# Kernel optimization log

Hardware: AMD Instinct MI355X
Metric: run time of the kernel (lower is better)

Reference implementation:

```python
import jax, jax.numpy as jnp
import numpy as np

# Static architecture of the decoded CNN (matches init_kwargs index_dict)
KERNEL_NO = [64, 128, 256]
KERNEL_SIZE = [9, 9, 9]
CH_IN = [3, 64, 128]
IDX_START = [0, 1792, 75648]
I_DIM = 370816  # last slice's last index + 1
D_MODEL = 512
BATCH = 128
N_LAYERS = len(KERNEL_NO)


def _build_slices():
    """Replicates DebedderNeuron.get_kernel_slices(); per-layer int32 index matrix [K_l, L_l]."""
    sl = []
    for idx in range(N_LAYERS):
        rows = []
        for kd in range(KERNEL_NO[idx]):
            s = IDX_START[idx] + kd * KERNEL_SIZE[idx] * CH_IN[idx]
            e = s + KERNEL_SIZE[idx] * CH_IN[idx]
            bias = IDX_START[idx] + KERNEL_NO[idx] * KERNEL_SIZE[idx] * CH_IN[idx] + kd
            ik = list(range(s, e)) + [bias]
            if idx < N_LAYERS - 1:
                for kn in range(KERNEL_NO[idx + 1]):
                    ns = (IDX_START[idx + 1] + kd * KERNEL_SIZE[idx + 1]
                          + kn * CH_IN[idx + 1] * KERNEL_SIZE[idx + 1])
                    ik.extend(range(ns, ns + KERNEL_SIZE[idx + 1]))
            rows.append(ik)
        sl.append(jnp.asarray(np.array(rows, dtype=np.int32)))
    return sl

IDX = _build_slices()  # lengths per row: [1180, 2881, 1153]


def setup_inputs() -> dict:
    key = jax.random.key(0)
    ks = jax.random.split(key, 7)
    dims = [int(IDX[l].shape[1]) for l in range(N_LAYERS)]
    inp = {"x": jax.random.normal(ks[0], (BATCH, sum(KERNEL_NO), D_MODEL), jnp.float32)}
    for l in range(N_LAYERS):
        inp[f"W{l}"] = jax.random.normal(ks[1 + 2 * l], (D_MODEL, dims[l]), jnp.float32) * 0.02
        inp[f"b{l}"] = jax.random.normal(ks[2 + 2 * l], (dims[l],), jnp.float32) * 0.02
    return inp


def reference(x, W0, b0, W1, b1, W2, b2):
    # One shared Linear per CNN layer (as in the torch module); batch all kernels of a
    # layer into a single GEMM, then scatter-add into the flat weight vector y.
    Ws = [W0, W1, W2]
    bs = [b0, b1, b2]
    y = jnp.zeros((x.shape[0], I_DIM), x.dtype)
    off = 0
    for l in range(N_LAYERS):
        K = KERNEL_NO[l]
        yt = jnp.einsum('bkd,di->bki', x[:, off:off + K], Ws[l]) + bs[l]  # [B, K_l, L_l]
        y = y.at[:, IDX[l]].add(yt)  # overlapping scatter-add, matches sequential += in torch
        off += K
    # middle layers are written twice (own slice + previous layer's extension) -> halve
    y = y.at[:, IDX_START[1]:IDX_START[-1]].multiply(0.5)
    return y
```

## Files before the change

### kernel.cpp

```cpp
#include <hip/hip_runtime.h>
#include <cstdint>

typedef short short8 __attribute__((ext_vector_type(8)));
typedef float f32x4 __attribute__((ext_vector_type(4)));

#define LDS_AS3(p) ((__attribute__((address_space(3))) unsigned*)(p))
#define GLB_AS1(p) ((const __attribute__((address_space(1))) unsigned*)(p))

__device__ inline unsigned bfpack(float a, float b) {
    union { float f; unsigned u; } ua, ub;
    ua.f = a; ub.f = b;
    unsigned lo = (ua.u + 0x7FFFu + ((ua.u >> 16) & 1u)) >> 16;
    unsigned hi = (ub.u + 0x7FFFu + ((ub.u >> 16) & 1u)) & 0xFFFF0000u;
    return lo | hi;
}

__global__ __launch_bounds__(256)
void cvt_x(const float* __restrict__ X, unsigned short* __restrict__ XB)
{
    const int g = blockIdx.x * 256 + threadIdx.x;
    const float4 v0 = *(const float4*)(X + (size_t)g * 8);
    const float4 v1 = *(const float4*)(X + (size_t)g * 8 + 4);
    uint4 u;
    u.x = bfpack(v0.x, v0.y); u.y = bfpack(v0.z, v0.w);
    u.z = bfpack(v1.x, v1.y); u.w = bfpack(v1.z, v1.w);
    *(uint4*)(XB + (size_t)g * 8) = u;
}

template <int N>
__global__ __launch_bounds__(256)
void cvt_w(const float* __restrict__ W, unsigned short* __restrict__ WT)
{
    const int g = blockIdx.x * 256 + threadIdx.x;
    if (g >= N * 64) return;
    const int n = g % N, d8 = g / N;
    const float* p = W + (size_t)d8 * 8 * N + n;
    uint4 u;
    u.x = bfpack(p[0],             p[(size_t)N]);
    u.y = bfpack(p[2 * (size_t)N], p[3 * (size_t)N]);
    u.z = bfpack(p[4 * (size_t)N], p[5 * (size_t)N]);
    u.w = bfpack(p[6 * (size_t)N], p[7 * (size_t)N]);
    *(uint4*)(WT + (size_t)n * 512 + d8 * 8) = u;
}

template <int MODE>
__global__ __launch_bounds__(256)
void gemm_scatter(const unsigned short* __restrict__ XB,
                  const unsigned short* __restrict__ WT,
                  const float* __restrict__ BIAS, float* __restrict__ Y)
{
    constexpr int K_L  = (MODE == 0) ? 64 : (MODE == 1) ? 128 : 256;
    constexpr int LOGK = (MODE == 0) ? 6  : (MODE == 1) ? 7   : 8;
    constexpr int N    = (MODE == 0) ? 1180 : (MODE == 1) ? 2881 : 1153;
    constexpr int XOFF = (MODE == 0) ? 0 : (MODE == 1) ? 64 : 192;
    constexpr int NT   = (N + 127) / 128;

    __shared__ __align__(16) unsigned short lA[2][128 * 32];
    __shared__ __align__(16) unsigned short lB[2][128 * 32];

    const int t    = threadIdx.x;
    const int lane = t & 63;
    const int wave = t >> 6;
    const int wr   = wave >> 1, wc = wave & 1;

    const int cpx = (int)gridDim.x >> 3;
    const int wg  = (blockIdx.x & 7) * cpx + (blockIdx.x >> 3);
    const int nt  = wg % NT;
    const int mt  = wg / NT;
    const int m0  = mt * 128;
    const int n0  = nt * 128;

    f32x4 acc[4][4] = {};

    auto stage = [&](int buf, int kk) {
        #pragma unroll
        for (int i = 0; i < 2; ++i) {
            const int cidx = i * 256 + t;
            const int row  = cidx >> 2;
            const int kgl  = (cidx & 3) ^ ((row >> 1) & 3);
            const int m    = m0 + row;
            const int b    = m >> LOGK;
            const int kd   = m & (K_L - 1);
            const unsigned short* gp =
                XB + ((size_t)(b * 448 + XOFF + kd) << 9) + kk + kgl * 8;
            __builtin_amdgcn_global_load_lds(GLB_AS1(gp), LDS_AS3(&lA[buf][cidx * 8]), 16, 0, 0);
        }
        #pragma unroll
        for (int i = 0; i < 2; ++i) {
            const int cidx = i * 256 + t;
            const int row  = cidx >> 2;
            const int kgl  = (cidx & 3) ^ ((row >> 1) & 3);
            int gc = n0 + row; if (gc > N - 1) gc = N - 1;
            const unsigned short* gp = WT + (size_t)gc * 512 + kk + kgl * 8;
            __builtin_amdgcn_global_load_lds(GLB_AS1(gp), LDS_AS3(&lB[buf][cidx * 8]), 16, 0, 0);
        }
    };

    stage(0, 0);
    __syncthreads();

    int cur = 0;
    #pragma unroll 1
    for (int ks = 0; ks < 16; ++ks) {
        const int nxt = cur ^ 1;
        if (ks < 15) stage(nxt, (ks + 1) * 32);

        const int kgl  = lane >> 4;
        const int lr16 = lane & 15;
        short8 af[4], bfr[4];
        #pragma unroll
        for (int mi = 0; mi < 4; ++mi) {
            const int row = wr * 64 + mi * 16 + lr16;
            af[mi] = *(const short8*)(&lA[cur][(row * 4 + (kgl ^ ((row >> 1) & 3))) * 8]);
        }
        #pragma unroll
        for (int ni = 0; ni < 4; ++ni) {
            const int row = wc * 64 + ni * 16 + lr16;
            bfr[ni] = *(const short8*)(&lB[cur][(row * 4 + (kgl ^ ((row >> 1) & 3))) * 8]);
        }
        #pragma unroll
        for (int mi = 0; mi < 4; ++mi)
            #pragma unroll
            for (int ni = 0; ni < 4; ++ni)
                acc[mi][ni] = __builtin_amdgcn_mfma_f32_16x16x32_bf16(
                    af[mi], bfr[ni], acc[mi][ni], 0, 0, 0);

        __syncthreads();
        cur = nxt;
    }

    const int lr = lane & 15;
    const int lq = lane >> 4;
    #pragma unroll
    for (int ni = 0; ni < 4; ++ni) {
        const int n = n0 + wc * 64 + ni * 16 + lr;
        if (n >= N) continue;
        const float bias = BIAS[n];
        #pragma unroll
        for (int mi = 0; mi < 4; ++mi) {
            #pragma unroll
            for (int r = 0; r < 4; ++r) {
                const int m  = m0 + wr * 64 + mi * 16 + lq * 4 + r;
                const int b  = m >> LOGK;
                const int kd = m & (K_L - 1);
                const float v = acc[mi][ni][r] + bias;
                float* yb = Y + (size_t)b * 370816;
                if (MODE == 0) {
                    if (n < 27)       yb[kd * 27 + n] = v;
                    else if (n == 27) yb[1728 + kd]   = v;
                    else {
                        int tt = n - 28, kn = tt / 9, j = tt - kn * 9;
                        yb[1792 + kn * 576 + kd * 9 + j] = 0.5f * v;
                    }
                } else if (MODE == 1) {
                    if (n < 576)       yb[1792 + kd * 576 + n] += 0.5f * v;
                    else if (n == 576) yb[75520 + kd] = 0.5f * v;
                    else {
                        int tt = n - 577, kn = tt / 9, j = tt - kn * 9;
                        yb[75648 + kn * 1152 + kd * 9 + j] = v;
                    }
                } else {
                    if (n < 1152) yb[75648 + kd * 1152 + n] += v;
                    else          yb[370560 + kd] = v;
                }
            }
        }
    }
}

extern "C" void kernel_launch(void* const* d_in, const int* in_sizes, int n_in,
                              void* d_out, int out_size, void* d_ws, size_t ws_size,
                              hipStream_t stream)
{
    const float* x  = (const float*)d_in[0];
    const float* W0 = (const float*)d_in[1];
    const float* b0 = (const float*)d_in[2];
    const float* W1 = (const float*)d_in[3];
    const float* b1 = (const float*)d_in[4];
    const float* W2 = (const float*)d_in[5];
    const float* b2 = (const float*)d_in[6];
    float* y = (float*)d_out;

    unsigned short* XB  = (unsigned short*)d_ws;
    unsigned short* WT0 = XB  + (size_t)128 * 448 * 512;
    unsigned short* WT1 = WT0 + (size_t)1180 * 512;
    unsigned short* WT2 = WT1 + (size_t)2881 * 512;

    cvt_x<<<dim3(14336), 256, 0, stream>>>(x, XB);
    cvt_w<1180><<<dim3((1180 * 64 + 255) / 256), 256, 0, stream>>>(W0, WT0);
    cvt_w<2881><<<dim3((2881 * 64 + 255) / 256), 256, 0, stream>>>(W1, WT1);
    cvt_w<1153><<<dim3((1153 * 64 + 255) / 256), 256, 0, stream>>>(W2, WT2);

    gemm_scatter<0><<<dim3(64 * 10),  256, 0, stream>>>(XB, WT0, b0, y);
    gemm_scatter<1><<<dim3(128 * 23), 256, 0, stream>>>(XB, WT1, b1, y);
    gemm_scatter<2><<<dim3(256 * 10), 256, 0, stream>>>(XB, WT2, b2, y);
}
```

Measured before the change: 308.2 us.

## Triple-buffer GEMM K-loop and stage overlap terms in bf16 scratch

Moves the K-loop from double to triple LDS buffering with explicit vmcnt waits and a single barrier per step, so global loads are issued two steps ahead. Also changes the epilogue: the overlapping extension outputs are no longer scattered into y and then read back with a read-modify-write. They are written contiguously as bf16 to workspace, and the next layer gathers them while writing y once. This removes the strided scatter and read-modify-write traffic on y but adds bf16 rounding of intermediate values and a gather read. The fused path needs enough workspace and falls back to the old epilogue otherwise.

Measured after the change: 302.2 us. No clear change (-1.9%).

```diff
diff --git a/kernel.cpp b/kernel.cpp
--- a/kernel.cpp
+++ b/kernel.cpp
@@ -13,6 +13,10 @@
     unsigned lo = (ua.u + 0x7FFFu + ((ua.u >> 16) & 1u)) >> 16;
     unsigned hi = (ub.u + 0x7FFFu + ((ub.u >> 16) & 1u)) & 0xFFFF0000u;
     return lo | hi;
+}
+__device__ inline unsigned short bf16of(float a) { return (unsigned short)bfpack(a, 0.0f); }
+__device__ inline float bf2f(unsigned short s) {
+    union { unsigned u; float f; } x; x.u = (unsigned)s << 16; return x.f;
 }
 
 __global__ __launch_bounds__(256)
@@ -43,11 +47,13 @@
     *(uint4*)(WT + (size_t)n * 512 + d8 * 8) = u;
 }
 
-template <int MODE>
+template <int MODE, bool FUSED>
 __global__ __launch_bounds__(256)
 void gemm_scatter(const unsigned short* __restrict__ XB,
                   const unsigned short* __restrict__ WT,
-                  const float* __restrict__ BIAS, float* __restrict__ Y)
+                  const float* __restrict__ BIAS, float* __restrict__ Y,
+                  const unsigned short* __restrict__ EXTI,
+                  unsigned short* __restrict__ EXTO)
 {
     constexpr int K_L  = (MODE == 0) ? 64 : (MODE == 1) ? 128 : 256;
     constexpr int LOGK = (MODE == 0) ? 6  : (MODE == 1) ? 7   : 8;
@@ -55,8 +61,8 @@
     constexpr int XOFF = (MODE == 0) ? 0 : (MODE == 1) ? 64 : 192;
     constexpr int NT   = (N + 127) / 128;
 
-    __shared__ __align__(16) unsigned short lA[2][128 * 32];
-    __shared__ __align__(16) unsigned short lB[2][128 * 32];
+    __shared__ __align__(16) unsigned short lA[3][128 * 32];
+    __shared__ __align__(16) unsigned short lB[3][128 * 32];
 
     const int t    = threadIdx.x;
     const int lane = t & 63;
@@ -97,13 +103,14 @@
     };
 
     stage(0, 0);
-    __syncthreads();
+    stage(1, 32);
 
     int cur = 0;
     #pragma unroll 1
     for (int ks = 0; ks < 16; ++ks) {
-        const int nxt = cur ^ 1;
-        if (ks < 15) stage(nxt, (ks + 1) * 32);
+        if (ks == 15) asm volatile("s_waitcnt vmcnt(0)" ::: "memory");
+        else          asm volatile("s_waitcnt vmcnt(4)" ::: "memory");
+        __builtin_amdgcn_s_barrier();
 
         const int kgl  = lane >> 4;
         const int lr16 = lane & 15;
@@ -118,6 +125,12 @@
             const int row = wc * 64 + ni * 16 + lr16;
             bfr[ni] = *(const short8*)(&lB[cur][(row * 4 + (kgl ^ ((row >> 1) & 3))) * 8]);
         }
+
+        if (ks < 14) {
+            int b2 = cur + 2; if (b2 >= 3) b2 -= 3;
+            stage(b2, (ks + 2) * 32);
+        }
+
         #pragma unroll
         for (int mi = 0; mi < 4; ++mi)
             #pragma unroll
@@ -125,8 +138,7 @@
                 acc[mi][ni] = __builtin_amdgcn_mfma_f32_16x16x32_bf16(
                     af[mi], bfr[ni], acc[mi][ni], 0, 0, 0);
 
-        __syncthreads();
-        cur = nxt;
+        cur = (cur + 1 == 3) ? 0 : cur + 1;
     }
 
     const int lr = lane & 15;
@@ -145,23 +157,42 @@
                 const int kd = m & (K_L - 1);
                 const float v = acc[mi][ni][r] + bias;
                 float* yb = Y + (size_t)b * 370816;
-                if (MODE == 0) {
-                    if (n < 27)       yb[kd * 27 + n] = v;
-                    else if (n == 27) yb[1728 + kd]   = v;
-                    else {
-                        int tt = n - 28, kn = tt / 9, j = tt - kn * 9;
-                        yb[1792 + kn * 576 + kd * 9 + j] = 0.5f * v;
-                    }
-                } else if (MODE == 1) {
-                    if (n < 576)       yb[1792 + kd * 576 + n] += 0.5f * v;
-                    else if (n == 576) yb[75520 + kd] = 0.5f * v;
-                    else {
-                        int tt = n - 577, kn = tt / 9, j = tt - kn * 9;
-                        yb[75648 + kn * 1152 + kd * 9 + j] = v;
+                if constexpr (FUSED) {
+                    if constexpr (MODE == 0) {
+                        if (n < 27)       yb[kd * 27 + n] = v;
+                        else if (n == 27) yb[1728 + kd]   = v;
+                        else EXTO[((size_t)(b * 64 + kd)) * 1152 + (n - 28)] = bf16of(v);
+                    } else if constexpr (MODE == 1) {
+                        if (n < 576) {
+                            const float e = bf2f(EXTI[((size_t)(b * 64 + n / 9)) * 1152 + kd * 9 + n % 9]);
+                            yb[1792 + kd * 576 + n] = 0.5f * (v + e);
+                        } else if (n == 576) yb[75520 + kd] = 0.5f * v;
+                        else EXTO[((size_t)(b * 128 + kd)) * 2304 + (n - 577)] = bf16of(v);
+                    } else {
+                        if (n < 1152) {
+                            const float e = bf2f(EXTI[((size_t)(b * 128 + n / 9)) * 2304 + kd * 9 + n % 9]);
+                            yb[75648 + kd * 1152 + n] = v + e;
+                        } else yb[370560 + kd] = v;
                     }
                 } else {
-                    if (n < 1152) yb[75648 + kd * 1152 + n] += v;
-                    else          yb[370560 + kd] = v;
+                    if constexpr (MODE == 0) {
+                        if (n < 27)       yb[kd * 27 + n] = v;
+                        else if (n == 27) yb[1728 + kd]   = v;
+                        else {
+                            int tt = n - 28, kn = tt / 9, j = tt - kn * 9;
+                            yb[1792 + kn * 576 + kd * 9 + j] = 0.5f * v;
+                        }
+                    } else if constexpr (MODE == 1) {
+                        if (n < 576)       yb[1792 + kd * 576 + n] += 0.5f * v;
+                        else if (n == 576) yb[75520 + kd] = 0.5f * v;
+                        else {
+                            int tt = n - 577, kn = tt / 9, j = tt - kn * 9;
+                            yb[75648 + kn * 1152 + kd * 9 + j] = v;
+                        }
+                    } else {
+                        if (n < 1152) yb[75648 + kd * 1152 + n] += v;
+                        else          yb[370560 + kd] = v;
+                    }
                 }
             }
         }
@@ -181,17 +212,28 @@
     const float* b2 = (const float*)d_in[6];
     float* y = (float*)d_out;
 
-    unsigned short* XB  = (unsigned short*)d_ws;
-    unsigned short* WT0 = XB  + (size_t)128 * 448 * 512;
-    unsigned short* WT1 = WT0 + (size_t)1180 * 512;
-    unsigned short* WT2 = WT1 + (size_t)2881 * 512;
+    unsigned short* XB   = (unsigned short*)d_ws;
+    unsigned short* WT0  = XB   + (size_t)128 * 448 * 512;
+    unsigned short* WT1  = WT0  + (size_t)1180 * 512;
+    unsigned short* WT2  = WT1  + (size_t)2881 * 512;
+    unsigned short* EXT0 = WT2  + (size_t)1153 * 512;
+    unsigned short* EXT1 = EXT0 + (size_t)128 * 64 * 1152;
+    const size_t NEED_FUSED =
+        ((size_t)128 * 448 * 512 + (size_t)5214 * 512 +
+         (size_t)128 * 64 * 1152 + (size_t)128 * 128 * 2304) * 2;
 
     cvt_x<<<dim3(14336), 256, 0, stream>>>(x, XB);
     cvt_w<1180><<<dim3((1180 * 64 + 255) / 256), 256, 0, stream>>>(W0, WT0);
     cvt_w<2881><<<dim3((2881 * 64 + 255) / 256), 256, 0, stream>>>(W1, WT1);
     cvt_w<1153><<<dim3((1153 * 64 + 255) / 256), 256, 0, stream>>>(W2, WT2);
 
-    gemm_scatter<0><<<dim3(64 * 10),  256, 0, stream>>>(XB, WT0, b0, y);
-    gemm_scatter<1><<<dim3(128 * 23), 256, 0, stream>>>(XB, WT1, b1, y);
-    gemm_scatter<2><<<dim3(256 * 10), 256, 0, stream>>>(XB, WT2, b2, y);
-}
+    if (ws_size >= NEED_FUSED) {
+        gemm_scatter<0, true><<<dim3(64 * 10),  256, 0, stream>>>(XB, WT0, b0, y, nullptr, EXT0);
+        gemm_scatter<1, true><<<dim3(128 * 23), 256, 0, stream>>>(XB, WT1, b1, y, EXT0, EXT1);
+        gemm_scatter<2, true><<<dim3(256 * 10), 256, 0, stream>>>(XB, WT2, b2, y, EXT1, nullptr);
+    } else {
+        gemm_scatter<0, false><<<dim3(64 * 10),  256, 0, stream>>>(XB, WT0, b0, y, nullptr, nullptr);
+        gemm_scatter<1, false><<<dim3(128 * 23), 256, 0, stream>>>(XB, WT1, b1, y, nullptr, nullptr);
+        gemm_scatter<2, false><<<dim3(256 * 10), 256, 0, stream>>>(XB, WT2, b2, y, nullptr, nullptr);
+    }
+}
```
